# Kernel tuning notes

Hardware: AMD Instinct MI355X
Metric: run time of the kernel (lower is better)

The kernel has to match this reference:

```python
import jax, jax.numpy as jnp
import numpy as np
import math

NUM_CLASSES = 80
MAX_ANCHOR_MATCHES = 10
ALPHA = 0.5
BETA = 6.0
EPSILON = 1e-9        # label-encoder epsilon
KEPS = 1e-7           # keras.backend.epsilon() used inside compute_ciou
B, NB = 16, 64        # batch, padded max GT boxes


def make_anchor_points():
    # YOLOv8 @ 640x640: strides 8/16/32 -> 80^2 + 40^2 + 20^2 = 8400 anchors
    pts = []
    for stride, n in [(8, 80), (16, 40), (32, 20)]:
        xs = (jnp.arange(n, dtype=jnp.float32) + 0.5) * stride
        gy, gx = jnp.meshgrid(xs, xs, indexing='ij')
        pts.append(jnp.stack([gx.reshape(-1), gy.reshape(-1)], axis=-1))
    return jnp.concatenate(pts, axis=0)  # (8400, 2)


def setup_inputs() -> dict:
    key = jax.random.key(0)
    k0, k1, k2, k3, k4, k5 = jax.random.split(key, 6)
    anc_points = make_anchor_points()
    NA = anc_points.shape[0]
    pd_scores = jax.random.uniform(k0, (B, NA, NUM_CLASSES), dtype=jnp.float32)
    # predicted boxes roughly centered on anchors
    wh = jax.random.uniform(k1, (B, NA, 2), minval=8.0, maxval=96.0)
    ctr = anc_points[None] + jax.random.normal(k2, (B, NA, 2)) * 8.0
    pd_bboxes = jnp.concatenate([ctr - wh / 2, ctr + wh / 2], axis=-1)
    # ground-truth boxes (xyxy) inside a 640x640 image
    g_wh = jax.random.uniform(k3, (B, NB, 2), minval=16.0, maxval=200.0)
    g_ctr = jax.random.uniform(k4, (B, NB, 2), minval=40.0, maxval=600.0)
    gt_bboxes = jnp.concatenate([g_ctr - g_wh / 2, g_ctr + g_wh / 2], axis=-1)
    gt_labels = jax.random.randint(k5, (B, NB), 0, NUM_CLASSES).astype(jnp.float32)
    # first 48 of 64 padded slots are real boxes
    mask_gt = jnp.broadcast_to(jnp.arange(NB)[None, :, None] < 48, (B, NB, 1))
    return {
        'pd_scores': pd_scores,
        'pd_bboxes': pd_bboxes,
        'anc_points': anc_points,
        'gt_labels': gt_labels,
        'gt_bboxes': gt_bboxes,
        'mask_gt': mask_gt,
    }


def compute_ciou(b1, b2):
    """CIoU between xyxy boxes b1 (gt) and b2 (pred); broadcasts, returns (...,)."""
    x1a, y1a, x2a, y2a = b1[..., 0], b1[..., 1], b1[..., 2], b1[..., 3]
    x1b, y1b, x2b, y2b = b2[..., 0], b2[..., 1], b2[..., 2], b2[..., 3]
    w1 = x2a - x1a
    h1 = y2a - y1a + KEPS
    w2 = x2b - x1b
    h2 = y2b - y1b + KEPS
    inter = (jnp.maximum(jnp.minimum(x2a, x2b) - jnp.maximum(x1a, x1b), 0.0)
             * jnp.maximum(jnp.minimum(y2a, y2b) - jnp.maximum(y1a, y1b), 0.0))
    union = w1 * h1 + w2 * h2 - inter + KEPS
    iou = inter / union
    cw = jnp.maximum(x2a, x2b) - jnp.minimum(x1a, x1b)
    ch = jnp.maximum(y2a, y2b) - jnp.minimum(y1a, y1b)
    c2 = cw * cw + ch * ch + KEPS
    rho2 = ((x1a + x2a) / 2 - (x1b + x2b) / 2) ** 2 + ((y1a + y2a) / 2 - (y1b + y2b) / 2) ** 2
    v = (4.0 / math.pi ** 2) * (jnp.arctan(w2 / h2) - jnp.arctan(w1 / h1)) ** 2
    alpha = v / (v - iou + (1.0 + KEPS))
    return iou - (rho2 / c2 + v * alpha)


def _encode(pd_scores, pd_bboxes, anc_points, gt_labels, gt_bboxes, mask_gt):
    Bn, NA, NC = pd_scores.shape
    NBn = gt_bboxes.shape[1]
    f32 = pd_scores.dtype
    mask_gt_b = mask_gt.astype(bool)                      # (B, NB, 1)

    # --- select_candidates_in_gts: anchor center inside gt box ---
    lt = gt_bboxes[:, :, None, :2]                        # (B, NB, 1, 2)
    rb = gt_bboxes[:, :, None, 2:]
    anc = anc_points[None, None, :, :]                    # (1, 1, NA, 2)
    deltas = jnp.concatenate([anc - lt, rb - anc], -1)    # (B, NB, NA, 4)
    mask_in_gts = jnp.min(deltas, axis=-1) > EPSILON      # (B, NB, NA)
    valid = mask_in_gts & mask_gt_b                       # (B, NB, NA)

    # --- get_box_metrics ---
    lbl = jnp.maximum(gt_labels.astype(jnp.int32), 0)     # (B, NB)
    sc = jnp.take_along_axis(pd_scores, jnp.broadcast_to(lbl[:, None, :], (Bn, NA, NBn)), axis=-1)
    sc = jnp.transpose(sc, (0, 2, 1))                     # (B, NB, NA)
    sc = jnp.where(gt_labels[:, :, None] >= 0, sc, 0.0)
    bbox_scores = jnp.where(valid, sc, 0.0)
    iou = compute_ciou(gt_bboxes[:, :, None, :], pd_bboxes[:, None, :, :])  # (B, NB, NA)
    iou = jnp.where(iou > 0, iou, 0.0)
    overlaps = jnp.where(valid, iou, 0.0)
    align_metric = jnp.power(bbox_scores, ALPHA) * jnp.power(overlaps, BETA)

    # --- select_topk_candidates ---
    k = MAX_ANCHOR_MATCHES
    _, topk_idxs = jax.lax.top_k(align_metric, k)         # (B, NB, k)
    topk_idxs = jnp.where(jnp.broadcast_to(mask_gt_b, (Bn, NBn, k)), topk_idxs, 0)
    bi = jnp.arange(Bn)[:, None, None]
    gi = jnp.arange(NBn)[None, :, None]
    counts = jnp.zeros((Bn, NBn, NA), f32).at[bi, gi, topk_idxs].add(1.0)
    mask_topk = jnp.where(counts > 1, 0.0, counts)        # drop idx-0 duplicates
    mask_pos = mask_topk * mask_in_gts.astype(f32) * mask_gt_b.astype(f32)

    # --- select_highest_overlaps (tie-break anchors matched to >1 gt) ---
    fg_mask = jnp.sum(mask_pos, axis=-2)                  # (B, NA)
    mask_multi = jnp.broadcast_to((fg_mask > 1)[:, None, :], (Bn, NBn, NA))
    max_idx = jnp.argmax(overlaps, axis=1)                # (B, NA)
    is_max = jnp.transpose(jax.nn.one_hot(max_idx, NBn, dtype=f32), (0, 2, 1))
    mask_pos = jnp.where(mask_multi, is_max, mask_pos)
    fg_mask = jnp.sum(mask_pos, axis=-2)
    target_gt_idx = jnp.argmax(mask_pos, axis=-2)         # (B, NA)

    # --- get_targets ---
    target_labels = jnp.take_along_axis(lbl, target_gt_idx, axis=1)          # (B, NA)
    target_bboxes = jnp.take_along_axis(gt_bboxes, target_gt_idx[..., None], axis=1)  # (B, NA, 4)
    target_scores = jax.nn.one_hot(target_labels, NC, dtype=f32)
    target_scores = jnp.where((fg_mask > 0)[..., None], target_scores, 0.0)

    # --- normalize class targets by alignment metric ---
    align_metric = align_metric * mask_pos
    pos_align = jnp.max(align_metric, axis=-1, keepdims=True)                # (B, NB, 1)
    pos_overlaps = jnp.max(overlaps * mask_pos, axis=-1, keepdims=True)
    norm = jnp.max(align_metric * pos_overlaps / (pos_align + EPSILON), axis=-2)[..., None]
    target_scores = target_scores * norm
    return target_bboxes, target_scores, fg_mask


def reference(pd_scores, pd_bboxes, anc_points, gt_labels, gt_bboxes, mask_gt):
    tb, ts, fg = _encode(pd_scores, pd_bboxes, anc_points, gt_labels, gt_bboxes, mask_gt)
    return (jax.lax.stop_gradient(tb), jax.lax.stop_gradient(ts), jax.lax.stop_gradient(fg))
```

## Files before the change

### kernel.cpp

```cpp
#include <hip/hip_runtime.h>
#include <cstdint>
#include <cstddef>

#define NBg 64
#define NCg 80
#define KTOP 10

__device__ __forceinline__ float ciou_dev(float gx1, float gy1, float gx2, float gy2,
                                          float px1, float py1, float px2, float py2) {
#pragma clang fp contract(off)
  const float keps = 1e-7f;
  float w1 = gx2 - gx1;
  float h1 = (gy2 - gy1) + keps;
  float w2 = px2 - px1;
  float h2 = (py2 - py1) + keps;
  float iw = fminf(gx2, px2) - fmaxf(gx1, px1);
  float ih = fminf(gy2, py2) - fmaxf(gy1, py1);
  float inter = fmaxf(iw, 0.0f) * fmaxf(ih, 0.0f);
  float uni = w1 * h1 + w2 * h2 - inter + keps;
  float iou = inter / uni;
  float cw = fmaxf(gx2, px2) - fminf(gx1, px1);
  float ch = fmaxf(gy2, py2) - fminf(gy1, py1);
  float c2 = cw * cw + ch * ch + keps;
  float dx = (gx1 + gx2) * 0.5f - (px1 + px2) * 0.5f;
  float dy = (gy1 + gy2) * 0.5f - (py1 + py2) * 0.5f;
  float rho2 = dx * dx + dy * dy;
  float q2 = w2 / h2;
  float q1 = w1 / h1;
  float t = (float)atan((double)q2) - (float)atan((double)q1);
  float v = 0.4052847345693511f * (t * t);
  float alpha = v / ((v - iou) + 1.0000001f);
  return iou - (rho2 / c2 + v * alpha);
}

__device__ __forceinline__ float am_dev(float sc, float ov) {
  float f1 = (float)sqrt((double)sc);
  double o = (double)ov;
  double o3 = o * o * o;
  return f1 * (float)(o3 * o3);
}

__global__ void ka_topk(const float* __restrict__ pd_scores,
                        const float* __restrict__ pd_bboxes,
                        const float* __restrict__ anc,
                        const float* __restrict__ gt_labels,
                        const float* __restrict__ gt_bboxes,
                        const int* __restrict__ mask_gt,
                        int* __restrict__ sel,
                        float* __restrict__ posAlign,
                        float* __restrict__ posOv,
                        int NA) {
  int row = blockIdx.x;
  int tid = threadIdx.x;
  int lane = tid & 63;
  int wid = tid >> 6;
  if (tid == 0) { posAlign[row] = 0.0f; posOv[row] = 0.0f; }
  if (!mask_gt[row]) {
    if (tid < KTOP) sel[row * KTOP + tid] = -1;
    return;
  }
  int b = row >> 6;
  const float* g = gt_bboxes + (size_t)row * 4;
  float gx1 = g[0], gy1 = g[1], gx2 = g[2], gy2 = g[3];
  float gl = gt_labels[row];
  int lbl = gl > 0.0f ? (int)gl : 0;
  bool glpos = (gl >= 0.0f);
  const float2* anc2 = (const float2*)anc;

  float v[KTOP];
  int id[KTOP];
#pragma unroll
  for (int k = 0; k < KTOP; k++) { v[k] = -1.0f; id[k] = 1 << 30; }

  auto ins = [&](float val, int a) {
    if (val > v[KTOP - 1] || (val == v[KTOP - 1] && a < id[KTOP - 1])) {
      v[KTOP - 1] = val; id[KTOP - 1] = a;
#pragma unroll
      for (int k = KTOP - 1; k > 0; k--) {
        bool sw = v[k] > v[k - 1] || (v[k] == v[k - 1] && id[k] < id[k - 1]);
        if (sw) {
          float tv = v[k]; v[k] = v[k - 1]; v[k - 1] = tv;
          int ti = id[k]; id[k] = id[k - 1]; id[k - 1] = ti;
        }
      }
    }
  };

  for (int a = tid; a < NA; a += 256) {
    float2 ap = anc2[a];
    float dmin = fminf(fminf(ap.x - gx1, ap.y - gy1),
                       fminf(gx2 - ap.x, gy2 - ap.y));
    float am = 0.0f;
    if (dmin > 1e-9f) {
      const float* pb = pd_bboxes + ((size_t)b * NA + a) * 4;
      float ci = ciou_dev(gx1, gy1, gx2, gy2, pb[0], pb[1], pb[2], pb[3]);
      float ov = ci > 0.0f ? ci : 0.0f;
      float sc = glpos ? pd_scores[((size_t)b * NA + a) * NCg + lbl] : 0.0f;
      am = am_dev(sc, ov);
    }
    ins(am, a);
  }

  float myval = 0.0f; int mysel = 0;
#pragma unroll
  for (int p = 0; p < KTOP; p++) {
    float bv = v[0]; int bi = id[0];
#pragma unroll
    for (int m = 1; m < 64; m <<= 1) {
      float ov_ = __shfl_xor(bv, m, 64);
      int oi = __shfl_xor(bi, m, 64);
      if (ov_ > bv || (ov_ == bv && oi < bi)) { bv = ov_; bi = oi; }
    }
    if (lane == p) { myval = bv; mysel = bi; }
    if (id[0] == bi) {
#pragma unroll
      for (int k = 0; k < KTOP - 1; k++) { v[k] = v[k + 1]; id[k] = id[k + 1]; }
      v[KTOP - 1] = -1.0f; id[KTOP - 1] = 1 << 30;
    }
  }

  __shared__ float lv[4 * KTOP];
  __shared__ int li[4 * KTOP];
  if (lane < KTOP) { lv[wid * KTOP + lane] = myval; li[wid * KTOP + lane] = mysel; }
  __syncthreads();
  if (wid != 0) return;

  float cv = (lane < 4 * KTOP) ? lv[lane] : -1.0f;
  int ci = (lane < 4 * KTOP) ? li[lane] : (1 << 30);
  int selw = 0;
#pragma unroll
  for (int p = 0; p < KTOP; p++) {
    float bv = cv; int bi = ci;
#pragma unroll
    for (int m = 1; m < 64; m <<= 1) {
      float ov_ = __shfl_xor(bv, m, 64);
      int oi = __shfl_xor(bi, m, 64);
      if (ov_ > bv || (ov_ == bv && oi < bi)) { bv = ov_; bi = oi; }
    }
    if (lane == p) selw = bi;
    if (ci == bi) { cv = -1.0f; ci = 1 << 30; }
  }

  if (lane < KTOP) {
    int a = selw;
    float2 ap = anc2[a];
    float dmin = fminf(fminf(ap.x - gx1, ap.y - gy1),
                       fminf(gx2 - ap.x, gy2 - ap.y));
    sel[row * KTOP + lane] = (dmin > 1e-9f) ? a : -1;
  }
}

__global__ void k3_resolve(const float* __restrict__ pd_scores,
                           const float* __restrict__ pd_bboxes,
                           const float* __restrict__ anc,
                           const float* __restrict__ gt_labels,
                           const float* __restrict__ gt_bboxes,
                           const int* __restrict__ mask_gt,
                           const int* __restrict__ sel,
                           int* __restrict__ tgt,
                           float* __restrict__ amv,
                           float* __restrict__ out_tb,
                           float* __restrict__ out_fg,
                           float* __restrict__ posAlign,
                           float* __restrict__ posOv,
                           int NA) {
  int b = blockIdx.y;
  int tid = threadIdx.x;
  int a0 = blockIdx.x * 256;
  int a = a0 + tid;
  __shared__ float4 sg[NBg];
  __shared__ int svalid[NBg];
  __shared__ int slbl[NBg];
  __shared__ int sglpos[NBg];
  __shared__ unsigned int mlo[256];
  __shared__ unsigned int mhi[256];
  mlo[tid] = 0u; mhi[tid] = 0u;
  if (tid < NBg) {
    int j = tid;
    const float* g = gt_bboxes + ((size_t)b * NBg + j) * 4;
    sg[j] = make_float4(g[0], g[1], g[2], g[3]);
    svalid[j] = mask_gt[b * NBg + j];
    float gl = gt_labels[b * NBg + j];
    slbl[j] = gl > 0.0f ? (int)gl : 0;
    sglpos[j] = (gl >= 0.0f) ? 1 : 0;
  }
  __syncthreads();
  for (int i = tid; i < NBg * KTOP; i += 256) {
    int e = sel[b * NBg * KTOP + i];
    int d = e - a0;
    if (d >= 0 && d < 256) {
      int j = i / KTOP;
      unsigned int bit = 1u << (j & 31);
      if (j < 32) atomicOr(&mlo[d], bit); else atomicOr(&mhi[d], bit);
    }
  }
  __syncthreads();
  if (a >= NA) return;
  unsigned int lo = mlo[tid], hi = mhi[tid];
  int cnt = __popc(lo) + __popc(hi);
  int first = lo ? (__ffs(lo) - 1) : (hi ? 32 + __ffs(hi) - 1 : 0);

  float ax = anc[2 * a], ay = anc[2 * a + 1];
  float px1 = 0.f, py1 = 0.f, px2 = 0.f, py2 = 0.f;
  if (cnt > 0) {
    const float* pb = pd_bboxes + ((size_t)b * NA + a) * 4;
    px1 = pb[0]; py1 = pb[1]; px2 = pb[2]; py2 = pb[3];
  }
  int t = 0;
  float fg = 0.0f;
  float ovt = -1.0f;
  if (cnt == 1) {
    t = first; fg = 1.0f;
  } else if (cnt > 1) {
    float best = -1.0f;
    for (int jj = 0; jj < NBg; jj++) {
      float ov = 0.0f;
      if (svalid[jj]) {
        float4 g = sg[jj];
        float dmin = fminf(fminf(ax - g.x, ay - g.y), fminf(g.z - ax, g.w - ay));
        if (dmin > 1e-9f) {
          float ci = ciou_dev(g.x, g.y, g.z, g.w, px1, py1, px2, py2);
          ov = ci > 0.0f ? ci : 0.0f;
        }
      }
      if (ov > best) { best = ov; t = jj; }
    }
    fg = 1.0f;
    ovt = best;
  }
  tgt[(size_t)b * NA + a] = t;
  out_fg[(size_t)b * NA + a] = fg;
  float4 gb = sg[t];
  ((float4*)out_tb)[(size_t)b * NA + a] = gb;
  float amval = 0.0f;
  if (fg > 0.0f) {
    float ov;
    if (ovt >= 0.0f) {
      ov = ovt;
    } else {
      float ci = ciou_dev(gb.x, gb.y, gb.z, gb.w, px1, py1, px2, py2);
      ov = ci > 0.0f ? ci : 0.0f;
    }
    float sc = sglpos[t] ? pd_scores[((size_t)b * NA + a) * NCg + slbl[t]] : 0.0f;
    amval = am_dev(sc, ov);
    atomicMax((int*)(posAlign + b * NBg + t), __float_as_int(amval));
    atomicMax((int*)(posOv + b * NBg + t), __float_as_int(ov));
  }
  amv[(size_t)b * NA + a] = amval;
}

__global__ void k5_scores(const float* __restrict__ gt_labels,
                          const int* __restrict__ tgt,
                          const float* __restrict__ out_fg,
                          const float* __restrict__ amv,
                          const float* __restrict__ posAlign,
                          const float* __restrict__ posOv,
                          float* __restrict__ out_ts,
                          int NA) {
  int b = blockIdx.y;
  int a0 = blockIdx.x * 256;
  int tid = threadIdx.x;
  int a = a0 + tid;
  __shared__ float snorm[256];
  __shared__ int slab[256];
  float norm = 0.0f;
  int lbl = -1;
  if (a < NA) {
    int t = tgt[(size_t)b * NA + a];
    float fg = out_fg[(size_t)b * NA + a];
    if (fg > 0.0f) {
      float av = amv[(size_t)b * NA + a];
      norm = av * posOv[b * NBg + t] / (posAlign[b * NBg + t] + 1e-9f);
      float gl = gt_labels[b * NBg + t];
      lbl = gl > 0.0f ? (int)gl : 0;
    }
  }
  snorm[tid] = norm;
  slab[tid] = lbl;
  __syncthreads();
  int nanch = NA - a0; if (nanch > 256) nanch = 256;
  int nf4 = nanch * (NCg / 4);
  float4* o = (float4*)(out_ts + ((size_t)b * NA + a0) * NCg);
  for (int i = tid; i < nf4; i += 256) {
    int aa = i / (NCg / 4);
    int c0 = (i % (NCg / 4)) * 4;
    int lb = slab[aa];
    float nv = snorm[aa];
    float4 w = make_float4(0.0f, 0.0f, 0.0f, 0.0f);
    int d = lb - c0;
    if (d >= 0 && d < 4) ((float*)&w)[d] = nv;
    o[i] = w;
  }
}

extern "C" void kernel_launch(void* const* d_in, const int* in_sizes, int n_in,
                              void* d_out, int out_size, void* d_ws, size_t ws_size,
                              hipStream_t stream) {
  const float* pd_scores = (const float*)d_in[0];
  const float* pd_bboxes = (const float*)d_in[1];
  const float* anc       = (const float*)d_in[2];
  const float* gt_labels = (const float*)d_in[3];
  const float* gt_bboxes = (const float*)d_in[4];
  const int*   mask_gt   = (const int*)d_in[5];

  int NA = in_sizes[2] / 2;
  int B  = in_sizes[3] / NBg;
  size_t nBA = (size_t)B * NA;

  float* out_tb = (float*)d_out;
  float* out_ts = out_tb + nBA * 4;
  float* out_fg = out_ts + nBA * NCg;

  char* ws = (char*)d_ws;
  size_t off = 0;
  int* sel = (int*)(ws + off);                off += (size_t)B * NBg * KTOP * 4;
  int* tgt = (int*)(ws + off);                off += nBA * 4;
  float* amv = (float*)(ws + off);            off += nBA * 4;
  float* posAlign = (float*)(ws + off);       off += (size_t)B * NBg * 4;
  float* posOv = (float*)(ws + off);          off += (size_t)B * NBg * 4;

  dim3 blk(256);
  int rows = B * NBg;
  ka_topk<<<rows, blk, 0, stream>>>(pd_scores, pd_bboxes, anc, gt_labels,
                                    gt_bboxes, mask_gt, sel, posAlign, posOv, NA);
  dim3 gA((NA + 255) / 256, B);
  k3_resolve<<<gA, blk, 0, stream>>>(pd_scores, pd_bboxes, anc, gt_labels,
                                     gt_bboxes, mask_gt, sel, tgt, amv,
                                     out_tb, out_fg, posAlign, posOv, NA);
  k5_scores<<<gA, blk, 0, stream>>>(gt_labels, tgt, out_fg, amv, posAlign, posOv,
                                    out_ts, NA);
}
```

Before: 180.0 us.

## Compact in-box anchors per wave and merge top-k via packed 64-bit keys

The top-k kernel now ballots each wave's anchors that fall inside the GT box into a shared-memory list and then runs the expensive CIoU/score work only over that compacted list. Previously every lane ran the heavy path divergently inside a strided loop. Candidates are packed as 64-bit keys (score bits plus inverted index), so each comparison is a single integer compare. The wave and block reductions become bitonic merges of 16-entry sorted lists instead of ten rounds of shuffle argmax. The cost is a 16 KB shared buffer and more registers for the 16-element key arrays, which may lower occupancy.

Measured after the change: 171.2 us. 4.9% less time.

```diff
diff --git a/kernel.cpp b/kernel.cpp
--- a/kernel.cpp
+++ b/kernel.cpp
@@ -5,6 +5,10 @@
 #define NBg 64
 #define NCg 80
 #define KTOP 10
+#define K16 16
+#define CAPW 1024
+
+typedef unsigned long long u64k;
 
 __device__ __forceinline__ float ciou_dev(float gx1, float gy1, float gx2, float gy2,
                                           float px1, float py1, float px2, float py2) {
@@ -40,6 +44,32 @@
   return f1 * (float)(o3 * o3);
 }
 
+__device__ __forceinline__ u64k mk_key(float am, int a) {
+  return ((u64k)__float_as_uint(am) << 32) | (unsigned)(~a);
+}
+
+__device__ __forceinline__ void merge16(u64k (&L)[K16], const u64k (&B)[K16]) {
+  u64k C[K16];
+#pragma unroll
+  for (int i = 0; i < K16; i++) {
+    u64k x = L[i], y = B[15 - i];
+    C[i] = x > y ? x : y;
+  }
+#pragma unroll
+  for (int s = 8; s > 0; s >>= 1) {
+#pragma unroll
+    for (int i = 0; i < K16; i++) {
+      if ((i & s) == 0) {
+        u64k x = C[i], y = C[i | s];
+        C[i] = x > y ? x : y;
+        C[i | s] = x > y ? y : x;
+      }
+    }
+  }
+#pragma unroll
+  for (int i = 0; i < K16; i++) L[i] = C[i];
+}
+
 __global__ void ka_topk(const float* __restrict__ pd_scores,
                         const float* __restrict__ pd_bboxes,
                         const float* __restrict__ anc,
@@ -67,86 +97,109 @@
   bool glpos = (gl >= 0.0f);
   const float2* anc2 = (const float2*)anc;
 
-  float v[KTOP];
-  int id[KTOP];
-#pragma unroll
-  for (int k = 0; k < KTOP; k++) { v[k] = -1.0f; id[k] = 1 << 30; }
-
-  auto ins = [&](float val, int a) {
-    if (val > v[KTOP - 1] || (val == v[KTOP - 1] && a < id[KTOP - 1])) {
-      v[KTOP - 1] = val; id[KTOP - 1] = a;
-#pragma unroll
-      for (int k = KTOP - 1; k > 0; k--) {
-        bool sw = v[k] > v[k - 1] || (v[k] == v[k - 1] && id[k] < id[k - 1]);
-        if (sw) {
-          float tv = v[k]; v[k] = v[k - 1]; v[k - 1] = tv;
-          int ti = id[k]; id[k] = id[k - 1]; id[k - 1] = ti;
-        }
+  __shared__ int slist[4 * CAPW];
+  __shared__ u64k xl[4][K16];
+
+  u64k k[KTOP];
+#pragma unroll
+  for (int q = 0; q < KTOP; q++) k[q] = 0;
+
+  auto ins = [&](u64k key) {
+    if (key > k[KTOP - 1]) {
+      k[KTOP - 1] = key;
+#pragma unroll
+      for (int q = KTOP - 1; q > 0; q--) {
+        if (k[q] > k[q - 1]) { u64k t = k[q]; k[q] = k[q - 1]; k[q - 1] = t; }
       }
     }
   };
 
-  for (int a = tid; a < NA; a += 256) {
-    float2 ap = anc2[a];
-    float dmin = fminf(fminf(ap.x - gx1, ap.y - gy1),
-                       fminf(gx2 - ap.x, gy2 - ap.y));
-    float am = 0.0f;
-    if (dmin > 1e-9f) {
-      const float* pb = pd_bboxes + ((size_t)b * NA + a) * 4;
-      float ci = ciou_dev(gx1, gy1, gx2, gy2, pb[0], pb[1], pb[2], pb[3]);
-      float ov = ci > 0.0f ? ci : 0.0f;
-      float sc = glpos ? pd_scores[((size_t)b * NA + a) * NCg + lbl] : 0.0f;
-      am = am_dev(sc, ov);
-    }
-    ins(am, a);
-  }
-
-  float myval = 0.0f; int mysel = 0;
-#pragma unroll
-  for (int p = 0; p < KTOP; p++) {
-    float bv = v[0]; int bi = id[0];
-#pragma unroll
-    for (int m = 1; m < 64; m <<= 1) {
-      float ov_ = __shfl_xor(bv, m, 64);
-      int oi = __shfl_xor(bi, m, 64);
-      if (ov_ > bv || (ov_ == bv && oi < bi)) { bv = ov_; bi = oi; }
-    }
-    if (lane == p) { myval = bv; mysel = bi; }
-    if (id[0] == bi) {
-#pragma unroll
-      for (int k = 0; k < KTOP - 1; k++) { v[k] = v[k + 1]; id[k] = id[k + 1]; }
-      v[KTOP - 1] = -1.0f; id[KTOP - 1] = 1 << 30;
-    }
-  }
-
-  __shared__ float lv[4 * KTOP];
-  __shared__ int li[4 * KTOP];
-  if (lane < KTOP) { lv[wid * KTOP + lane] = myval; li[wid * KTOP + lane] = mysel; }
-  __syncthreads();
-  if (wid != 0) return;
-
-  float cv = (lane < 4 * KTOP) ? lv[lane] : -1.0f;
-  int ci = (lane < 4 * KTOP) ? li[lane] : (1 << 30);
-  int selw = 0;
-#pragma unroll
-  for (int p = 0; p < KTOP; p++) {
-    float bv = cv; int bi = ci;
-#pragma unroll
-    for (int m = 1; m < 64; m <<= 1) {
-      float ov_ = __shfl_xor(bv, m, 64);
-      int oi = __shfl_xor(bi, m, 64);
-      if (ov_ > bv || (ov_ == bv && oi < bi)) { bv = ov_; bi = oi; }
-    }
-    if (lane == p) selw = bi;
-    if (ci == bi) { cv = -1.0f; ci = 1 << 30; }
-  }
-
-  if (lane < KTOP) {
-    int a = selw;
-    float2 ap = anc2[a];
-    float dmin = fminf(fminf(ap.x - gx1, ap.y - gy1),
-                       fminf(gx2 - ap.x, gy2 - ap.y));
-    sel[row * KTOP + lane] = (dmin > 1e-9f) ? a : -1;
+  auto heavy = [&](int a) {
+    const float4 pb = ((const float4*)pd_bboxes)[(size_t)b * NA + a];
+    float ci = ciou_dev(gx1, gy1, gx2, gy2, pb.x, pb.y, pb.z, pb.w);
+    float ov = ci > 0.0f ? ci : 0.0f;
+    float sc = glpos ? pd_scores[((size_t)b * NA + a) * NCg + lbl] : 0.0f;
+    ins(mk_key(am_dev(sc, ov), a));
+  };
+
+  int wcnt = 0;
+  u64k lmask_lt = (1ull << lane) - 1;
+#pragma unroll
+  for (int itb = 0; itb < 9; itb++) {
+    float2 p[4];
+    int idx[4];
+#pragma unroll
+    for (int u = 0; u < 4; u++) {
+      idx[u] = tid + (itb * 4 + u) * 256;
+      p[u] = (idx[u] < NA) ? anc2[idx[u]] : make_float2(0.0f, 0.0f);
+    }
+#pragma unroll
+    for (int u = 0; u < 4; u++) {
+      bool valid = idx[u] < NA;
+      float dmin = fminf(fminf(p[u].x - gx1, p[u].y - gy1),
+                         fminf(gx2 - p[u].x, gy2 - p[u].y));
+      bool inbox = valid && (dmin > 1e-9f);
+      u64k m = __ballot(inbox);
+      if (inbox) {
+        int pos = wcnt + __popcll(m & lmask_lt);
+        if (pos < CAPW) slist[wid * CAPW + pos] = idx[u];
+        else heavy(idx[u]);
+      } else if (valid) {
+        ins((u64k)(unsigned)(~idx[u]));
+      }
+      wcnt += __popcll(m);
+    }
+  }
+  int wslots = wcnt < CAPW ? wcnt : CAPW;
+
+  for (int i = lane; i < wslots; i += 64) heavy(slist[wid * CAPW + i]);
+
+  u64k L[K16];
+#pragma unroll
+  for (int q = 0; q < KTOP; q++) L[q] = k[q];
+#pragma unroll
+  for (int q = KTOP; q < K16; q++) L[q] = 0;
+
+#pragma unroll
+  for (int step = 0; step < 6; step++) {
+    u64k B[K16];
+#pragma unroll
+    for (int q = 0; q < K16; q++)
+      B[q] = __shfl_xor((unsigned long long)L[q], 1 << step, 64);
+    merge16(L, B);
+  }
+
+  if (lane < K16) xl[wid][lane] = L[lane];
+  __syncthreads();
+  if (wid == 2) {
+    u64k B[K16];
+#pragma unroll
+    for (int q = 0; q < K16; q++) B[q] = xl[3][q];
+    merge16(L, B);
+    if (lane < K16) xl[2][lane] = L[lane];
+  }
+  if (wid == 0) {
+    u64k B[K16];
+#pragma unroll
+    for (int q = 0; q < K16; q++) B[q] = xl[1][q];
+    merge16(L, B);
+  }
+  __syncthreads();
+  if (wid == 0) {
+    u64k B[K16];
+#pragma unroll
+    for (int q = 0; q < K16; q++) B[q] = xl[2][q];
+    merge16(L, B);
+    if (lane == 0) {
+#pragma unroll
+      for (int q = 0; q < KTOP; q++) {
+        int a = ~((unsigned)L[q]);
+        float2 ap = anc2[a];
+        float dmin = fminf(fminf(ap.x - gx1, ap.y - gy1),
+                           fminf(gx2 - ap.x, gy2 - ap.y));
+        sel[row * KTOP + q] = (dmin > 1e-9f) ? a : -1;
+      }
+    }
   }
 }
 
```
